# Performance work log

Measured on AMD Instinct MI355X. Metric: run time of the kernel, lower is better.

## Reference

```python
import jax, jax.numpy as jnp
import numpy as np

N = 10000      # nodes
E = 160000     # edges
D_IN = 512
D_H = 512
P_DROP = 0.2


def _glorot(key, shape):
    lim = float(np.sqrt(6.0 / (shape[0] + shape[1])))
    return jax.random.uniform(key, shape, jnp.float32, -lim, lim)


def setup_inputs() -> dict:
    key = jax.random.key(0)
    ks = jax.random.split(key, 8)
    h = jax.random.normal(ks[0], (N, D_IN), jnp.float32)
    src = jax.random.randint(ks[1], (E,), 0, N)
    dst = jax.random.randint(ks[2], (E,), 0, N)
    edge_weight = jax.random.uniform(ks[3], (E,), jnp.float32)
    W0 = _glorot(ks[4], (D_IN, D_H))
    W1 = _glorot(ks[5], (D_H, D_H))
    W2 = _glorot(ks[6], (D_H, D_H))
    b0 = jnp.zeros((D_H,), jnp.float32)
    b1 = jnp.zeros((D_H,), jnp.float32)
    b2 = jnp.zeros((D_H,), jnp.float32)
    return dict(h=h, src=src, dst=dst, edge_weight=edge_weight,
                W0=W0, b0=b0, W1=W1, b1=b1, W2=W2, b2=b2)


def _dropout(x, key):
    keep = jax.random.bernoulli(key, 1.0 - P_DROP, x.shape)
    return jnp.where(keep, x / (1.0 - P_DROP), 0.0)


def _graph_conv(x, src, dst, ew, W, b, act):
    # DGL GraphConv, norm='both', weight=True, bias=True, with edge_weight.
    ones = jnp.ones((src.shape[0],), x.dtype)
    deg_out = jnp.maximum(jax.ops.segment_sum(ones, src, num_segments=N), 1.0)
    deg_in = jnp.maximum(jax.ops.segment_sum(ones, dst, num_segments=N), 1.0)
    x = x * (deg_out ** -0.5)[:, None]          # src norm
    msg = x[src] * ew[:, None]                  # [E, D] gather + edge weight
    agg = jax.ops.segment_sum(msg, dst, num_segments=N)  # scatter-add
    out = (agg @ W) * (deg_in ** -0.5)[:, None] + b
    return act(out) if act is not None else out


def reference(h, src, dst, edge_weight, W0, b0, W1, b1, W2, b2):
    dk = jax.random.split(jax.random.key(42), 3)
    x = _dropout(h, dk[0])
    x = _graph_conv(x, src, dst, edge_weight, W0, b0, jax.nn.elu)
    x = _dropout(x, dk[1])
    x = _graph_conv(x, src, dst, edge_weight, W1, b1, jax.nn.elu)
    x = _dropout(x, dk[2])
    x = _graph_conv(x, src, dst, edge_weight, W2, b2, None)
    return x
```

## Files before the change

### kernel.cpp

```cpp
#include <hip/hip_runtime.h>
#include <stdint.h>

#define N_NODES 10000
#define N_EDGES 160000
#define D 512
#define TOT (N_NODES * D)
#define M_PAD 10112

typedef _Float16 h8 __attribute__((ext_vector_type(8)));
typedef float f4 __attribute__((ext_vector_type(4)));

__host__ __device__ inline uint32_t rotl32(uint32_t v, int r) {
    return (v << r) | (v >> (32 - r));
}

__host__ __device__ inline void tf2x32(uint32_t k0, uint32_t k1,
                                       uint32_t& x0, uint32_t& x1) {
    uint32_t k2 = k0 ^ k1 ^ 0x1BD11BDAu;
    x0 += k0; x1 += k1;
    x0 += x1; x1 = rotl32(x1, 13); x1 ^= x0;
    x0 += x1; x1 = rotl32(x1, 15); x1 ^= x0;
    x0 += x1; x1 = rotl32(x1, 26); x1 ^= x0;
    x0 += x1; x1 = rotl32(x1,  6); x1 ^= x0;
    x0 += k1; x1 += k2 + 1u;
    x0 += x1; x1 = rotl32(x1, 17); x1 ^= x0;
    x0 += x1; x1 = rotl32(x1, 29); x1 ^= x0;
    x0 += x1; x1 = rotl32(x1, 16); x1 ^= x0;
    x0 += x1; x1 = rotl32(x1, 24); x1 ^= x0;
    x0 += k2; x1 += k0 + 2u;
    x0 += x1; x1 = rotl32(x1, 13); x1 ^= x0;
    x0 += x1; x1 = rotl32(x1, 15); x1 ^= x0;
    x0 += x1; x1 = rotl32(x1, 26); x1 ^= x0;
    x0 += x1; x1 = rotl32(x1,  6); x1 ^= x0;
    x0 += k0; x1 += k1 + 3u;
    x0 += x1; x1 = rotl32(x1, 17); x1 ^= x0;
    x0 += x1; x1 = rotl32(x1, 29); x1 ^= x0;
    x0 += x1; x1 = rotl32(x1, 16); x1 ^= x0;
    x0 += x1; x1 = rotl32(x1, 24); x1 ^= x0;
    x0 += k1; x1 += k2 + 4u;
    x0 += x1; x1 = rotl32(x1, 13); x1 ^= x0;
    x0 += x1; x1 = rotl32(x1, 15); x1 ^= x0;
    x0 += x1; x1 = rotl32(x1, 26); x1 ^= x0;
    x0 += x1; x1 = rotl32(x1,  6); x1 ^= x0;
    x0 += k2; x1 += k0 + 5u;
}

__device__ __forceinline__ float dropout_gate(uint32_t k0, uint32_t k1, uint32_t j) {
    uint32_t c0 = 0u, c1 = j;
    tf2x32(k0, k1, c0, c1);
    uint32_t bits = c0 ^ c1;
    float u = __uint_as_float((bits >> 9) | 0x3f800000u) - 1.0f;
    return (u < 0.8f) ? 1.0f : 0.0f;
}

__global__ void hist_kernel(const int* __restrict__ src, const int* __restrict__ dst,
                            int* __restrict__ deg_out, int* __restrict__ deg_in) {
    int e = blockIdx.x * 256 + threadIdx.x;
    if (e >= N_EDGES) return;
    atomicAdd(&deg_out[src[e]], 1);
    atomicAdd(&deg_in[dst[e]], 1);
}

__global__ __launch_bounds__(1024)
void scan_kernel(const int* __restrict__ deg_in, const int* __restrict__ deg_out,
                 int* __restrict__ row_ptr,
                 float* __restrict__ rn_in, float* __restrict__ rn_out) {
    __shared__ int wsum[16];
    __shared__ int base_s;
    int tid = threadIdx.x;
    int lane = tid & 63, wv = tid >> 6;
    if (tid == 0) base_s = 0;
    __syncthreads();
    for (int start = 0; start < N_NODES; start += 1024) {
        int i = start + tid;
        int v = (i < N_NODES) ? deg_in[i] : 0;
        int s = v;
#pragma unroll
        for (int off = 1; off < 64; off <<= 1) {
            int t = __shfl_up(s, off, 64);
            if (lane >= off) s += t;
        }
        if (lane == 63) wsum[wv] = s;
        __syncthreads();
        if (wv == 0 && lane < 16) {
            int ws = wsum[lane];
#pragma unroll
            for (int off = 1; off < 16; off <<= 1) {
                int t = __shfl_up(ws, off, 64);
                if (lane >= off) ws += t;
            }
            wsum[lane] = ws;
        }
        __syncthreads();
        if (i < N_NODES) {
            int prefix = base_s + ((wv > 0) ? wsum[wv - 1] : 0) + (s - v);
            row_ptr[i] = prefix;
            rn_in[i]  = 1.0f / sqrtf(fmaxf((float)v, 1.0f));
            rn_out[i] = 1.0f / sqrtf(fmaxf((float)deg_out[i], 1.0f));
        }
        __syncthreads();
        if (tid == 0) base_s += wsum[15];
        __syncthreads();
    }
    if (tid == 0) row_ptr[N_NODES] = base_s;
}

__global__ void fill_kernel(const int* __restrict__ src, const int* __restrict__ dst,
                            const float* __restrict__ ew, const int* __restrict__ row_ptr,
                            int* __restrict__ cursor, int2* __restrict__ csr) {
    int e = blockIdx.x * 256 + threadIdx.x;
    if (e >= N_EDGES) return;
    int v = dst[e];
    int pos = atomicAdd(&cursor[v], 1);
    int idx = row_ptr[v] + pos;
    csr[idx] = make_int2(src[e], __float_as_int(ew[e]));
}

__global__ __launch_bounds__(256)
void wconvert_kernel(const float* __restrict__ W0, const float* __restrict__ W1,
                     const float* __restrict__ W2, _Float16* __restrict__ Wt) {
    __shared__ float tile[64][65];
    const float* W = (blockIdx.z == 0) ? W0 : (blockIdx.z == 1) ? W1 : W2;
    _Float16* T = Wt + (size_t)blockIdx.z * 512 * 512;
    int r0 = blockIdx.y * 64, c0 = blockIdx.x * 64;
    int t = threadIdx.x;
    int c = t & 63, rq = t >> 6;
#pragma unroll
    for (int i = 0; i < 16; ++i) {
        int r = rq + i * 4;
        tile[r][c] = W[(size_t)(r0 + r) * 512 + c0 + c];
    }
    __syncthreads();
    int k = t & 63, nq = t >> 6;
#pragma unroll
    for (int i = 0; i < 16; ++i) {
        int n = nq + i * 4;
        T[(size_t)(c0 + n) * 512 + r0 + k] = (_Float16)tile[k][n];
    }
}

__global__ __launch_bounds__(256)
void dropout_kernel(const float* __restrict__ x, _Float16* __restrict__ y,
                    const float* __restrict__ rn_out, uint32_t k0, uint32_t k1) {
    int t = blockIdx.x * 256 + threadIdx.x;
    int j = t * 4;
    if (j >= TOT) return;
    float4 xv = *(const float4*)&x[j];
    float w = rn_out[j >> 9];
    _Float16 r[4];
    uint32_t jj = (uint32_t)j;
#pragma unroll
    for (int i = 0; i < 4; ++i) {
        float g = dropout_gate(k0, k1, jj + (uint32_t)i);
        float xi = (&xv.x)[i];
        r[i] = (_Float16)(g * (xi / 0.8f) * w);
    }
    *(ushort4*)&y[j] = *(ushort4*)r;
}

__global__ __launch_bounds__(256)
void aggregate_kernel(const _Float16* __restrict__ y, const int* __restrict__ row_ptr,
                      const int2* __restrict__ csr, _Float16* __restrict__ agg) {
    int node = blockIdx.x * 4 + (threadIdx.x >> 6);
    int lane = threadIdx.x & 63;
    if (node >= N_NODES) return;
    int beg = row_ptr[node], end = row_ptr[node + 1];
    float acc[8] = {0, 0, 0, 0, 0, 0, 0, 0};
    int k = beg;
    for (; k + 3 < end; k += 4) {
        int2 e0 = csr[k], e1 = csr[k + 1], e2 = csr[k + 2], e3 = csr[k + 3];
        h8 a0 = *(const h8*)&y[(size_t)e0.x * 512 + lane * 8];
        h8 a1 = *(const h8*)&y[(size_t)e1.x * 512 + lane * 8];
        h8 a2 = *(const h8*)&y[(size_t)e2.x * 512 + lane * 8];
        h8 a3 = *(const h8*)&y[(size_t)e3.x * 512 + lane * 8];
        float w0 = __int_as_float(e0.y), w1 = __int_as_float(e1.y);
        float w2 = __int_as_float(e2.y), w3 = __int_as_float(e3.y);
#pragma unroll
        for (int i = 0; i < 8; ++i)
            acc[i] += w0 * (float)a0[i] + w1 * (float)a1[i]
                    + w2 * (float)a2[i] + w3 * (float)a3[i];
    }
    for (; k < end; ++k) {
        int2 e0 = csr[k];
        float w0 = __int_as_float(e0.y);
        h8 a = *(const h8*)&y[(size_t)e0.x * 512 + lane * 8];
#pragma unroll
        for (int i = 0; i < 8; ++i) acc[i] += w0 * (float)a[i];
    }
    _Float16 r[8];
#pragma unroll
    for (int i = 0; i < 8; ++i) r[i] = (_Float16)acc[i];
    *(h8*)&agg[(size_t)node * 512 + lane * 8] = *(h8*)r;
}

#define GBK 32
#define LDA 40
__global__ __launch_bounds__(256)
void gemm_kernel(const _Float16* __restrict__ A, const _Float16* __restrict__ Wt,
                 const float* __restrict__ bias, const float* __restrict__ rn_in,
                 const float* __restrict__ rn_out,
                 _Float16* __restrict__ yout, float* __restrict__ fout,
                 int mode, uint32_t k0, uint32_t k1) {
    __shared__ _Float16 As[128 * LDA];
    __shared__ _Float16 Bs[64 * LDA];
    int tid = threadIdx.x;
    int wv = tid >> 6, lane = tid & 63;

    int f = blockIdx.x + blockIdx.y * 8;
    int T = (f & 7) * 79 + (f >> 3);
    int row0 = (T >> 3) * 128, col0 = (T & 7) * 64;

    int wr = wv >> 1, wc = wv & 1;

    f4 acc[4][2];
#pragma unroll
    for (int i = 0; i < 4; ++i)
#pragma unroll
        for (int j = 0; j < 2; ++j) acc[i][j] = (f4){0.f, 0.f, 0.f, 0.f};

    int srow = tid >> 2;
    int sseg = (tid & 3) * 8;
    const _Float16* gA0 = A + (size_t)(row0 + srow) * 512 + sseg;
    const _Float16* gA1 = gA0 + (size_t)64 * 512;
    const _Float16* gB  = Wt + (size_t)(col0 + srow) * 512 + sseg;
    _Float16* wA0 = &As[srow * LDA + sseg];
    _Float16* wA1 = &As[(64 + srow) * LDA + sseg];
    _Float16* wB  = &Bs[srow * LDA + sseg];

    int kf = (lane >> 4) * 8;
    const _Float16* fa = &As[(wr * 64 + (lane & 15)) * LDA + kf];
    const _Float16* fb = &Bs[(wc * 32 + (lane & 15)) * LDA + kf];

    h8 ra0 = *(const h8*)gA0;
    h8 ra1 = *(const h8*)gA1;
    h8 rb  = *(const h8*)gB;

    for (int kk = 0; kk < 512; kk += GBK) {
        *(h8*)wA0 = ra0;
        *(h8*)wA1 = ra1;
        *(h8*)wB  = rb;
        __syncthreads();
        if (kk + GBK < 512) {
            ra0 = *(const h8*)(gA0 + kk + GBK);
            ra1 = *(const h8*)(gA1 + kk + GBK);
            rb  = *(const h8*)(gB  + kk + GBK);
        }
        h8 af[4], bf[2];
#pragma unroll
        for (int mt = 0; mt < 4; ++mt) af[mt] = *(const h8*)(fa + mt * 16 * LDA);
#pragma unroll
        for (int nt = 0; nt < 2; ++nt) bf[nt] = *(const h8*)(fb + nt * 16 * LDA);
#pragma unroll
        for (int mt = 0; mt < 4; ++mt)
#pragma unroll
            for (int nt = 0; nt < 2; ++nt)
                acc[mt][nt] = __builtin_amdgcn_mfma_f32_16x16x32_f16(
                    af[mt], bf[nt], acc[mt][nt], 0, 0, 0);
        __syncthreads();
    }

    int mbase = row0 + wr * 64;
    int nbase = col0 + wc * 32;
#pragma unroll
    for (int mt = 0; mt < 4; ++mt) {
#pragma unroll
        for (int nt = 0; nt < 2; ++nt) {
            int gr0 = mbase + mt * 16 + (lane >> 4) * 4;
            int gc = nbase + nt * 16 + (lane & 15);
            float bcol = bias[gc];
#pragma unroll
            for (int i = 0; i < 4; ++i) {
                int gr = gr0 + i;
                if (gr >= N_NODES) continue;
                float v = acc[mt][nt][i] * rn_in[gr] + bcol;
                if (mode == 0) {
                    v = (v > 0.f) ? v : expm1f(v);
                    float g = dropout_gate(k0, k1, (uint32_t)(gr * 512 + gc));
                    v = g * (v / 0.8f) * rn_out[gr];
                    yout[(size_t)gr * 512 + gc] = (_Float16)v;
                } else {
                    fout[(size_t)gr * 512 + gc] = v;
                }
            }
        }
    }
}

extern "C" void kernel_launch(void* const* d_in, const int* in_sizes, int n_in,
                              void* d_out, int out_size, void* d_ws, size_t ws_size,
                              hipStream_t stream) {
    const float* h   = (const float*)d_in[0];
    const int*   src = (const int*)d_in[1];
    const int*   dst = (const int*)d_in[2];
    const float* ew  = (const float*)d_in[3];
    const float* W0  = (const float*)d_in[4];
    const float* b0  = (const float*)d_in[5];
    const float* W1  = (const float*)d_in[6];
    const float* b1  = (const float*)d_in[7];
    const float* W2  = (const float*)d_in[8];
    const float* b2  = (const float*)d_in[9];
    const float* bl[3] = {b0, b1, b2};
    float* out = (float*)d_out;

    char* ws = (char*)d_ws;
    _Float16* y16  = (_Float16*)ws; ws += (size_t)TOT * 2;
    _Float16* aggF = (_Float16*)ws; ws += (size_t)M_PAD * 512 * 2;
    _Float16* Wt   = (_Float16*)ws; ws += (size_t)3 * 512 * 512 * 2;
    int* degi_in  = (int*)ws;  ws += N_NODES * 4;
    int* degi_out = (int*)ws;  ws += N_NODES * 4;
    int* cursor   = (int*)ws;  ws += N_NODES * 4;
    int* row_ptr  = (int*)ws;  ws += (N_NODES + 1) * 4;
    ws = (char*)(((uintptr_t)ws + 15) & ~(uintptr_t)15);
    int2* csr     = (int2*)ws; ws += (size_t)N_EDGES * 8;
    float* rn_in  = (float*)ws; ws += N_NODES * 4;
    float* rn_out = (float*)ws; ws += N_NODES * 4;

    hipMemsetAsync(degi_in, 0, 3 * N_NODES * 4, stream);

    hist_kernel<<<(N_EDGES + 255) / 256, 256, 0, stream>>>(src, dst, degi_out, degi_in);
    scan_kernel<<<1, 1024, 0, stream>>>(degi_in, degi_out, row_ptr, rn_in, rn_out);
    fill_kernel<<<(N_EDGES + 255) / 256, 256, 0, stream>>>(src, dst, ew, row_ptr,
                                                           cursor, csr);
    wconvert_kernel<<<dim3(8, 8, 3), 256, 0, stream>>>(W0, W1, W2, Wt);

    uint32_t dk[3][2];
    for (int i = 0; i < 3; ++i) {
        uint32_t c0 = 0u, c1 = (uint32_t)i;
        tf2x32(0u, 42u, c0, c1);
        dk[i][0] = c0; dk[i][1] = c1;
    }

    dropout_kernel<<<(TOT / 4 + 255) / 256, 256, 0, stream>>>(h, y16, rn_out,
                                                              dk[0][0], dk[0][1]);
    for (int l = 0; l < 3; ++l) {
        aggregate_kernel<<<N_NODES / 4, 256, 0, stream>>>(y16, row_ptr, csr, aggF);
        int mode = (l < 2) ? 0 : 1;
        uint32_t dk0 = (l < 2) ? dk[l + 1][0] : 0u;
        uint32_t dk1 = (l < 2) ? dk[l + 1][1] : 0u;
        gemm_kernel<<<dim3(8, M_PAD / 128), 256, 0, stream>>>(
            aggF, Wt + (size_t)l * 512 * 512, bl[l], rn_in, rn_out,
            y16, out, mode, dk0, dk1);
    }
}
```

Before: 308.9 us.

## Unfuse dropout from GEMM epilogue, load B fragments directly, widen aggregate unroll

Moves the inter-layer dropout and source normalization out of the GEMM epilogue into a separate fp16 elementwise kernel that reads an intermediate buffer. The GEMM now loads B fragments straight from global memory into registers instead of staging them through shared memory. The aggregation loop is unrolled to eight edges so more gathers are in flight. The trade-off is an extra kernel launch and a full extra read and write of the activation per layer, plus uncoalesced B loads in the GEMM.

```diff
diff --git a/kernel.cpp b/kernel.cpp
--- a/kernel.cpp
+++ b/kernel.cpp
@@ -159,6 +159,24 @@
 }
 
 __global__ __launch_bounds__(256)
+void dropout16_kernel(const _Float16* __restrict__ x, _Float16* __restrict__ y,
+                      const float* __restrict__ rn_out, uint32_t k0, uint32_t k1) {
+    int t = blockIdx.x * 256 + threadIdx.x;
+    int j = t * 8;
+    if (j >= TOT) return;
+    h8 xv = *(const h8*)&x[j];
+    float w = rn_out[j >> 9];
+    _Float16 r[8];
+    uint32_t jj = (uint32_t)j;
+#pragma unroll
+    for (int i = 0; i < 8; ++i) {
+        float g = dropout_gate(k0, k1, jj + (uint32_t)i);
+        r[i] = (_Float16)(g * ((float)xv[i] / 0.8f) * w);
+    }
+    *(h8*)&y[j] = *(h8*)r;
+}
+
+__global__ __launch_bounds__(256)
 void aggregate_kernel(const _Float16* __restrict__ y, const int* __restrict__ row_ptr,
                       const int2* __restrict__ csr, _Float16* __restrict__ agg) {
     int node = blockIdx.x * 4 + (threadIdx.x >> 6);
@@ -167,18 +185,33 @@
     int beg = row_ptr[node], end = row_ptr[node + 1];
     float acc[8] = {0, 0, 0, 0, 0, 0, 0, 0};
     int k = beg;
+    for (; k + 7 < end; k += 8) {
+        h8 a[8];
+        float w[8];
+#pragma unroll
+        for (int q = 0; q < 8; ++q) {
+            int2 e = csr[k + q];
+            a[q] = *(const h8*)&y[(size_t)e.x * 512 + lane * 8];
+            w[q] = __int_as_float(e.y);
+        }
+#pragma unroll
+        for (int q = 0; q < 8; ++q)
+#pragma unroll
+            for (int i = 0; i < 8; ++i) acc[i] += w[q] * (float)a[q][i];
+    }
     for (; k + 3 < end; k += 4) {
-        int2 e0 = csr[k], e1 = csr[k + 1], e2 = csr[k + 2], e3 = csr[k + 3];
-        h8 a0 = *(const h8*)&y[(size_t)e0.x * 512 + lane * 8];
-        h8 a1 = *(const h8*)&y[(size_t)e1.x * 512 + lane * 8];
-        h8 a2 = *(const h8*)&y[(size_t)e2.x * 512 + lane * 8];
-        h8 a3 = *(const h8*)&y[(size_t)e3.x * 512 + lane * 8];
-        float w0 = __int_as_float(e0.y), w1 = __int_as_float(e1.y);
-        float w2 = __int_as_float(e2.y), w3 = __int_as_float(e3.y);
-#pragma unroll
-        for (int i = 0; i < 8; ++i)
-            acc[i] += w0 * (float)a0[i] + w1 * (float)a1[i]
-                    + w2 * (float)a2[i] + w3 * (float)a3[i];
+        h8 a[4];
+        float w[4];
+#pragma unroll
+        for (int q = 0; q < 4; ++q) {
+            int2 e = csr[k + q];
+            a[q] = *(const h8*)&y[(size_t)e.x * 512 + lane * 8];
+            w[q] = __int_as_float(e.y);
+        }
+#pragma unroll
+        for (int q = 0; q < 4; ++q)
+#pragma unroll
+            for (int i = 0; i < 8; ++i) acc[i] += w[q] * (float)a[q][i];
     }
     for (; k < end; ++k) {
         int2 e0 = csr[k];
@@ -198,11 +231,8 @@
 __global__ __launch_bounds__(256)
 void gemm_kernel(const _Float16* __restrict__ A, const _Float16* __restrict__ Wt,
                  const float* __restrict__ bias, const float* __restrict__ rn_in,
-                 const float* __restrict__ rn_out,
-                 _Float16* __restrict__ yout, float* __restrict__ fout,
-                 int mode, uint32_t k0, uint32_t k1) {
+                 _Float16* __restrict__ yout, float* __restrict__ fout, int mode) {
     __shared__ _Float16 As[128 * LDA];
-    __shared__ _Float16 Bs[64 * LDA];
     int tid = threadIdx.x;
     int wv = tid >> 6, lane = tid & 63;
 
@@ -222,40 +252,40 @@
     int sseg = (tid & 3) * 8;
     const _Float16* gA0 = A + (size_t)(row0 + srow) * 512 + sseg;
     const _Float16* gA1 = gA0 + (size_t)64 * 512;
-    const _Float16* gB  = Wt + (size_t)(col0 + srow) * 512 + sseg;
     _Float16* wA0 = &As[srow * LDA + sseg];
     _Float16* wA1 = &As[(64 + srow) * LDA + sseg];
-    _Float16* wB  = &Bs[srow * LDA + sseg];
 
     int kf = (lane >> 4) * 8;
     const _Float16* fa = &As[(wr * 64 + (lane & 15)) * LDA + kf];
-    const _Float16* fb = &Bs[(wc * 32 + (lane & 15)) * LDA + kf];
+    const _Float16* gB0 = Wt + (size_t)(col0 + wc * 32 + (lane & 15)) * 512 + kf;
+    const _Float16* gB1 = gB0 + (size_t)16 * 512;
 
     h8 ra0 = *(const h8*)gA0;
     h8 ra1 = *(const h8*)gA1;
-    h8 rb  = *(const h8*)gB;
+    h8 rb0 = *(const h8*)gB0;
+    h8 rb1 = *(const h8*)gB1;
 
     for (int kk = 0; kk < 512; kk += GBK) {
         *(h8*)wA0 = ra0;
         *(h8*)wA1 = ra1;
-        *(h8*)wB  = rb;
+        h8 bf0 = rb0, bf1 = rb1;
         __syncthreads();
         if (kk + GBK < 512) {
             ra0 = *(const h8*)(gA0 + kk + GBK);
             ra1 = *(const h8*)(gA1 + kk + GBK);
-            rb  = *(const h8*)(gB  + kk + GBK);
-        }
-        h8 af[4], bf[2];
+            rb0 = *(const h8*)(gB0 + kk + GBK);
+            rb1 = *(const h8*)(gB1 + kk + GBK);
+        }
+        h8 af[4];
 #pragma unroll
         for (int mt = 0; mt < 4; ++mt) af[mt] = *(const h8*)(fa + mt * 16 * LDA);
 #pragma unroll
-        for (int nt = 0; nt < 2; ++nt) bf[nt] = *(const h8*)(fb + nt * 16 * LDA);
-#pragma unroll
-        for (int mt = 0; mt < 4; ++mt)
-#pragma unroll
-            for (int nt = 0; nt < 2; ++nt)
-                acc[mt][nt] = __builtin_amdgcn_mfma_f32_16x16x32_f16(
-                    af[mt], bf[nt], acc[mt][nt], 0, 0, 0);
+        for (int mt = 0; mt < 4; ++mt) {
+            acc[mt][0] = __builtin_amdgcn_mfma_f32_16x16x32_f16(af[mt], bf0,
+                                                                acc[mt][0], 0, 0, 0);
+            acc[mt][1] = __builtin_amdgcn_mfma_f32_16x16x32_f16(af[mt], bf1,
+                                                                acc[mt][1], 0, 0, 0);
+        }
         __syncthreads();
     }
 
@@ -275,8 +305,6 @@
                 float v = acc[mt][nt][i] * rn_in[gr] + bcol;
                 if (mode == 0) {
                     v = (v > 0.f) ? v : expm1f(v);
-                    float g = dropout_gate(k0, k1, (uint32_t)(gr * 512 + gc));
-                    v = g * (v / 0.8f) * rn_out[gr];
                     yout[(size_t)gr * 512 + gc] = (_Float16)v;
                 } else {
                     fout[(size_t)gr * 512 + gc] = v;
@@ -304,6 +332,7 @@
 
     char* ws = (char*)d_ws;
     _Float16* y16  = (_Float16*)ws; ws += (size_t)TOT * 2;
+    _Float16* yPre = (_Float16*)ws; ws += (size_t)TOT * 2;
     _Float16* aggF = (_Float16*)ws; ws += (size_t)M_PAD * 512 * 2;
     _Float16* Wt   = (_Float16*)ws; ws += (size_t)3 * 512 * 512 * 2;
     int* degi_in  = (int*)ws;  ws += N_NODES * 4;
@@ -335,10 +364,11 @@
     for (int l = 0; l < 3; ++l) {
         aggregate_kernel<<<N_NODES / 4, 256, 0, stream>>>(y16, row_ptr, csr, aggF);
         int mode = (l < 2) ? 0 : 1;
-        uint32_t dk0 = (l < 2) ? dk[l + 1][0] : 0u;
-        uint32_t dk1 = (l < 2) ? dk[l + 1][1] : 0u;
         gemm_kernel<<<dim3(8, M_PAD / 128), 256, 0, stream>>>(
-            aggF, Wt + (size_t)l * 512 * 512, bl[l], rn_in, rn_out,
-            y16, out, mode, dk0, dk1);
-    }
-}
+            aggF, Wt + (size_t)l * 512 * 512, bl[l], rn_in, yPre, out, mode);
+        if (l < 2) {
+            dropout16_kernel<<<TOT / 8 / 256, 256, 0, stream>>>(
+                yPre, y16, rn_out, dk[l + 1][0], dk[l + 1][1]);
+        }
+    }
+}
```

New measurement: 319.6 us. 3.5% more time.
